# Kernel tuning notes

Measured on AMD Instinct MI355X. Metric: run time of the kernel, lower is better.

## Reference

```python
import jax, jax.numpy as jnp
import numpy as np

N_NODES = 100_000
N_EDGES = 3_200_000
IN_DIM, HID, OUT_DIM = 500, 16, 500


def _gcn_conv(x, W, b, src, dst, norm, n_nodes):
    # PyG GCNConv: h = X W; out[dst] += norm * h[src]; out += b
    h = x @ W                                   # [N, out]
    msg = h[src] * norm[:, None]                # [E+N, out]
    out = jax.ops.segment_sum(msg, dst, num_segments=n_nodes)
    return out + b


def setup_inputs() -> dict:
    key = jax.random.key(0)
    ks = jax.random.split(key, 8)
    x = jax.random.normal(ks[0], (N_NODES, IN_DIM), dtype=jnp.float32)
    edge_index = jax.random.randint(ks[1], (2, N_EDGES), 0, N_NODES, dtype=jnp.int32)
    # Glorot-ish init scale for the linear weights
    W1 = jax.random.normal(ks[2], (IN_DIM, HID), dtype=jnp.float32) * (1.0 / np.sqrt(IN_DIM))
    b1 = jnp.zeros((HID,), dtype=jnp.float32)
    W2 = jax.random.normal(ks[3], (HID, HID), dtype=jnp.float32) * (1.0 / np.sqrt(HID))
    b2 = jnp.zeros((HID,), dtype=jnp.float32)
    W3 = jax.random.normal(ks[4], (HID, OUT_DIM), dtype=jnp.float32) * (1.0 / np.sqrt(HID))
    b3 = jnp.zeros((OUT_DIM,), dtype=jnp.float32)
    return {"x": x, "edge_index": edge_index, "W1": W1, "b1": b1,
            "W2": W2, "b2": b2, "W3": W3, "b3": b3}


def reference(x, edge_index, W1, b1, W2, b2, W3, b3):
    n = x.shape[0]
    loops = jnp.arange(n, dtype=edge_index.dtype)
    src = jnp.concatenate([edge_index[0], loops])  # add self-loops
    dst = jnp.concatenate([edge_index[1], loops])
    # symmetric normalization: deg over (A + I), norm_e = d^-1/2[src] * d^-1/2[dst]
    deg = jax.ops.segment_sum(jnp.ones_like(src, dtype=x.dtype), dst, num_segments=n)
    dis = jnp.where(deg > 0, jax.lax.rsqrt(deg), 0.0)
    norm = dis[src] * dis[dst]

    h = _gcn_conv(x, W1, b1, src, dst, norm, n)
    h = jax.nn.relu(h)
    h = _gcn_conv(h, W2, b2, src, dst, norm, n)
    h = jax.nn.relu(h)
    out = _gcn_conv(h, W3, b3, src, dst, norm, n)
    return out
```

## Files before the change

### kernel.cpp

```cpp
#include <hip/hip_runtime.h>

#define N_NODES 100000
#define N_EDGES 3200000
#define IN_DIM 500
#define HID 16
#define OUT_DIM 500

__global__ void k_deg(const int* __restrict__ dst, int* __restrict__ cnt, int E) {
    int e = blockIdx.x * blockDim.x + threadIdx.x;
    if (e < E) atomicAdd(&cnt[dst[e]], 1);
}

__global__ void k_dis(const int* __restrict__ cnt, float* __restrict__ dis, int n) {
    int i = blockIdx.x * blockDim.x + threadIdx.x;
    if (i < n) dis[i] = rsqrtf((float)(cnt[i] + 1));
}

__global__ __launch_bounds__(1024) void k_scanA(const int* __restrict__ cnt,
                                                int* __restrict__ rowptr,
                                                int* __restrict__ bsum) {
    __shared__ int sh[1024];
    int t = threadIdx.x;
    int i = blockIdx.x * 1024 + t;
    int v = (i < N_NODES) ? cnt[i] : 0;
    sh[t] = v;
    __syncthreads();
    for (int off = 1; off < 1024; off <<= 1) {
        int tmp = (t >= off) ? sh[t - off] : 0;
        __syncthreads();
        sh[t] += tmp;
        __syncthreads();
    }
    if (i < N_NODES) rowptr[i] = sh[t] - v;
    if (t == 1023) bsum[blockIdx.x] = sh[1023];
}

__global__ __launch_bounds__(128) void k_scanB(int* __restrict__ bsum, int nb) {
    __shared__ int sh[128];
    int t = threadIdx.x;
    int v = (t < nb) ? bsum[t] : 0;
    sh[t] = v;
    __syncthreads();
    for (int off = 1; off < 128; off <<= 1) {
        int tmp = (t >= off) ? sh[t - off] : 0;
        __syncthreads();
        sh[t] += tmp;
        __syncthreads();
    }
    if (t < nb) bsum[t] = sh[t] - v;
}

__global__ void k_scanC(int* __restrict__ rowptr, const int* __restrict__ bsum) {
    int i = blockIdx.x * blockDim.x + threadIdx.x;
    if (i < N_NODES) rowptr[i] += bsum[i >> 10];
    if (i == 0) rowptr[N_NODES] = N_EDGES;
}

__global__ void k_fill(const int* __restrict__ src, const int* __restrict__ dst,
                       const int* __restrict__ rowptr, int* __restrict__ cursor,
                       int* __restrict__ csr, int E) {
    int e = blockIdx.x * blockDim.x + threadIdx.x;
    if (e < E) {
        int d = dst[e];
        int p = rowptr[d] + atomicAdd(&cursor[d], 1);
        csr[p] = src[e];
    }
}

__global__ __launch_bounds__(256) void k_mm1(const float* __restrict__ x,
                                             const float* __restrict__ W,
                                             const float* __restrict__ dis,
                                             float* __restrict__ hp) {
    int row = blockIdx.x * 256 + threadIdx.x;
    if (row >= N_NODES) return;
    const float4* xr = (const float4*)(x + (size_t)row * IN_DIM);
    float acc[HID];
#pragma unroll
    for (int j = 0; j < HID; ++j) acc[j] = 0.0f;

    float4 A[8], B[8];
#pragma unroll
    for (int m = 0; m < 8; ++m) A[m] = xr[m];

#define MM1_GROUP(buf, g)                                                 \
    {                                                                     \
        const float* Wg = W + (size_t)(g) * 32 * HID;                     \
        _Pragma("unroll") for (int m = 0; m < 8; ++m) {                   \
            float4 a = buf[m];                                            \
            _Pragma("unroll") for (int j = 0; j < HID; ++j) {             \
                acc[j] += a.x * Wg[(4 * m + 0) * HID + j]                 \
                        + a.y * Wg[(4 * m + 1) * HID + j]                 \
                        + a.z * Wg[(4 * m + 2) * HID + j]                 \
                        + a.w * Wg[(4 * m + 3) * HID + j];                \
            }                                                             \
        }                                                                 \
    }

    for (int gg = 0; gg < 7; ++gg) {
        int g0 = 2 * gg;
#pragma unroll
        for (int m = 0; m < 8; ++m) B[m] = xr[8 * (g0 + 1) + m];
        MM1_GROUP(A, g0);
#pragma unroll
        for (int m = 0; m < 8; ++m) A[m] = xr[8 * (g0 + 2) + m];
        MM1_GROUP(B, g0 + 1);
    }
    MM1_GROUP(A, 14);
#pragma unroll
    for (int m = 0; m < 5; ++m) {
        float4 a = xr[120 + m];
        const float* Wg = W + (size_t)(480 + 4 * m) * HID;
#pragma unroll
        for (int j = 0; j < HID; ++j) {
            acc[j] += a.x * Wg[j] + a.y * Wg[HID + j] +
                      a.z * Wg[2 * HID + j] + a.w * Wg[3 * HID + j];
        }
    }
#undef MM1_GROUP

    float di = dis[row];
    float4* hr = (float4*)(hp + (size_t)row * HID);
#pragma unroll
    for (int q = 0; q < 4; ++q)
        hr[q] = make_float4(di * acc[4 * q + 0], di * acc[4 * q + 1],
                            di * acc[4 * q + 2], di * acc[4 * q + 3]);
}

__global__ __launch_bounds__(256) void k_mm2(const float* __restrict__ o,
                                             const float* __restrict__ W,
                                             const float* __restrict__ dis,
                                             float* __restrict__ hp) {
    int row = blockIdx.x * 256 + threadIdx.x;
    if (row >= N_NODES) return;
    const float4* orow = (const float4*)(o + (size_t)row * HID);
    float av[HID];
#pragma unroll
    for (int q = 0; q < 4; ++q) {
        float4 a = orow[q];
        av[4 * q + 0] = a.x; av[4 * q + 1] = a.y;
        av[4 * q + 2] = a.z; av[4 * q + 3] = a.w;
    }
    float acc[HID];
#pragma unroll
    for (int j = 0; j < HID; ++j) acc[j] = 0.0f;
#pragma unroll
    for (int k = 0; k < HID; ++k) {
#pragma unroll
        for (int j = 0; j < HID; ++j) acc[j] += av[k] * W[k * HID + j];
    }
    float di = dis[row];
    float4* hr = (float4*)(hp + (size_t)row * HID);
#pragma unroll
    for (int q = 0; q < 4; ++q)
        hr[q] = make_float4(di * acc[4 * q + 0], di * acc[4 * q + 1],
                            di * acc[4 * q + 2], di * acc[4 * q + 3]);
}

__global__ void k_scale(const float* __restrict__ o, const float* __restrict__ dis,
                        float* __restrict__ hp) {
    int t = blockIdx.x * blockDim.x + threadIdx.x;
    if (t < N_NODES * HID) hp[t] = dis[t >> 4] * o[t];
}

template <int RELU>
__global__ __launch_bounds__(256) void k_gather(const int* __restrict__ rowptr,
                                                const int* __restrict__ csr,
                                                const float* __restrict__ dis,
                                                const float* __restrict__ hp,
                                                const float* __restrict__ b,
                                                float* __restrict__ o) {
    int g = threadIdx.x >> 4;
    int f = threadIdx.x & 15;
    int d = blockIdx.x * 16 + g;
    int start = rowptr[d];
    int end = rowptr[d + 1];
    float s = 0.0f;
    for (int e0 = start; e0 < end; e0 += 16) {
        int idx = e0 + f;
        int sid = (idx < end) ? csr[idx] : 0;
        int m = end - e0;
        if (m > 16) m = 16;
        for (int j = 0; j < m; ++j) {
            int sj = __shfl(sid, j, 16);
            s += hp[(size_t)sj * HID + f];
        }
    }
    float di = dis[d];
    float v = di * (s + hp[(size_t)d * HID + f]);
    if (RELU) {
        v += b[f];
        v = v > 0.0f ? v : 0.0f;
    }
    o[(size_t)d * HID + f] = v;
}

__global__ __launch_bounds__(256) void k_mm3(const float* __restrict__ a,
                                             const float* __restrict__ W,
                                             const float* __restrict__ b,
                                             float* __restrict__ out) {
    __shared__ float Ws[HID * OUT_DIM];
    __shared__ float bs[OUT_DIM];
    for (int t = threadIdx.x; t < HID * OUT_DIM; t += 256) Ws[t] = W[t];
    for (int t = threadIdx.x; t < OUT_DIM; t += 256) bs[t] = b[t];
    __syncthreads();
    int ct = threadIdx.x & 127;
    int rt = threadIdx.x >> 7;
    int r0 = blockIdx.x * 8 + rt * 4;
    float areg[4][16];
#pragma unroll
    for (int rr = 0; rr < 4; ++rr) {
        const float4* ap = (const float4*)(a + (size_t)(r0 + rr) * HID);
        float4 v0 = ap[0], v1 = ap[1], v2 = ap[2], v3 = ap[3];
        areg[rr][0] = v0.x;  areg[rr][1] = v0.y;  areg[rr][2] = v0.z;  areg[rr][3] = v0.w;
        areg[rr][4] = v1.x;  areg[rr][5] = v1.y;  areg[rr][6] = v1.z;  areg[rr][7] = v1.w;
        areg[rr][8] = v2.x;  areg[rr][9] = v2.y;  areg[rr][10] = v2.z; areg[rr][11] = v2.w;
        areg[rr][12] = v3.x; areg[rr][13] = v3.y; areg[rr][14] = v3.z; areg[rr][15] = v3.w;
    }
    if (ct >= 125) return;
    int j0 = ct * 4;
    float acc[4][4];
#pragma unroll
    for (int rr = 0; rr < 4; ++rr) {
        acc[rr][0] = bs[j0];
        acc[rr][1] = bs[j0 + 1];
        acc[rr][2] = bs[j0 + 2];
        acc[rr][3] = bs[j0 + 3];
    }
#pragma unroll
    for (int k = 0; k < HID; ++k) {
        float4 w = *(const float4*)&Ws[k * OUT_DIM + j0];
#pragma unroll
        for (int rr = 0; rr < 4; ++rr) {
            acc[rr][0] += areg[rr][k] * w.x;
            acc[rr][1] += areg[rr][k] * w.y;
            acc[rr][2] += areg[rr][k] * w.z;
            acc[rr][3] += areg[rr][k] * w.w;
        }
    }
#pragma unroll
    for (int rr = 0; rr < 4; ++rr) {
        float4 r = make_float4(acc[rr][0], acc[rr][1], acc[rr][2], acc[rr][3]);
        *(float4*)&out[(size_t)(r0 + rr) * OUT_DIM + j0] = r;
    }
}

extern "C" void kernel_launch(void* const* d_in, const int* in_sizes, int n_in,
                              void* d_out, int out_size, void* d_ws, size_t ws_size,
                              hipStream_t stream) {
    const float* x  = (const float*)d_in[0];
    const int* ei   = (const int*)d_in[1];
    const float* W1 = (const float*)d_in[2];
    const float* b1 = (const float*)d_in[3];
    const float* W2 = (const float*)d_in[4];
    const float* b2 = (const float*)d_in[5];
    const float* W3 = (const float*)d_in[6];
    const float* b3 = (const float*)d_in[7];
    float* out = (float*)d_out;

    const int* src = ei;
    const int* dst = ei + N_EDGES;

    char* w = (char*)d_ws;
    float* dis    = (float*)(w);
    int*   cnt    = (int*)(w + 401408);
    int*   rowptr = (int*)(w + 802816);
    int*   bsum   = (int*)(w + 1205248);
    int*   csr    = (int*)(w + 1205760);
    float* hp     = (float*)(w + 14005760);
    float* o      = (float*)(w + 20405760);

    const int B = 256;
    int gN   = (N_NODES + B - 1) / B;
    int gE   = (N_EDGES + B - 1) / B;
    int gNH  = (N_NODES * HID + B - 1) / B;
    int gG   = N_NODES / 16;
    int gMM3 = N_NODES / 8;
    int gScanA = (N_NODES + 1023) / 1024;

    hipMemsetAsync(cnt, 0, N_NODES * sizeof(int), stream);
    k_deg<<<gE, B, 0, stream>>>(dst, cnt, N_EDGES);
    k_dis<<<gN, B, 0, stream>>>(cnt, dis, N_NODES);

    k_scanA<<<gScanA, 1024, 0, stream>>>(cnt, rowptr, bsum);
    k_scanB<<<1, 128, 0, stream>>>(bsum, gScanA);
    k_scanC<<<gN, B, 0, stream>>>(rowptr, bsum);
    hipMemsetAsync(cnt, 0, N_NODES * sizeof(int), stream);
    k_fill<<<gE, B, 0, stream>>>(src, dst, rowptr, cnt, csr, N_EDGES);

    k_mm1<<<gN, B, 0, stream>>>(x, W1, dis, hp);
    k_gather<1><<<gG, B, 0, stream>>>(rowptr, csr, dis, hp, b1, o);

    k_mm2<<<gN, B, 0, stream>>>(o, W2, dis, hp);
    k_gather<1><<<gG, B, 0, stream>>>(rowptr, csr, dis, hp, b2, o);

    k_scale<<<gNH, B, 0, stream>>>(o, dis, hp);
    k_gather<0><<<gG, B, 0, stream>>>(rowptr, csr, dis, hp, b3, o);
    k_mm3<<<gMM3, B, 0, stream>>>(o, W3, b3, out);
}
```

Before: 937.2 us.

## Build CSR with a two-pass bucketed sort instead of global atomic scatter

```diff
diff --git a/kernel.cpp b/kernel.cpp
--- a/kernel.cpp
+++ b/kernel.cpp
@@ -5,6 +5,10 @@
 #define IN_DIM 500
 #define HID 16
 #define OUT_DIM 500
+
+#define BSHIFT 9
+#define NBUCK 196
+#define PLACE_CAP 24576
 
 __global__ void k_deg(const int* __restrict__ dst, int* __restrict__ cnt, int E) {
     int e = blockIdx.x * blockDim.x + threadIdx.x;
@@ -56,14 +60,86 @@
     if (i == 0) rowptr[N_NODES] = N_EDGES;
 }
 
-__global__ void k_fill(const int* __restrict__ src, const int* __restrict__ dst,
-                       const int* __restrict__ rowptr, int* __restrict__ cursor,
-                       int* __restrict__ csr, int E) {
-    int e = blockIdx.x * blockDim.x + threadIdx.x;
-    if (e < E) {
-        int d = dst[e];
-        int p = rowptr[d] + atomicAdd(&cursor[d], 1);
-        csr[p] = src[e];
+__global__ void k_initcur(const int* __restrict__ rowptr, int* __restrict__ cur) {
+    int b = blockIdx.x * blockDim.x + threadIdx.x;
+    if (b < NBUCK) cur[b] = rowptr[b << BSHIFT];
+}
+
+__global__ __launch_bounds__(512) void k_bin(const int* __restrict__ src,
+                                             const int* __restrict__ dst,
+                                             int* __restrict__ cur,
+                                             unsigned* __restrict__ ebin, int E) {
+    __shared__ int hist[NBUCK];
+    __shared__ int gbase[NBUCK];
+    int t = threadIdx.x;
+    for (int i = t; i < NBUCK; i += 512) hist[i] = 0;
+    __syncthreads();
+    int base = blockIdx.x * 8192;
+    unsigned epack[16];
+    unsigned lpack[16];
+#pragma unroll
+    for (int q = 0; q < 16; ++q) {
+        int e = base + q * 512 + t;
+        unsigned ep = 0, lp = 0xFFFFFFFFu;
+        if (e < E) {
+            int s = src[e];
+            int d = dst[e];
+            int b = d >> BSHIFT;
+            int loc = atomicAdd(&hist[b], 1);
+            ep = ((unsigned)s << BSHIFT) | (unsigned)(d & 511);
+            lp = ((unsigned)loc << 8) | (unsigned)b;
+        }
+        epack[q] = ep;
+        lpack[q] = lp;
+    }
+    __syncthreads();
+    for (int i = t; i < NBUCK; i += 512)
+        gbase[i] = hist[i] ? atomicAdd(&cur[i], hist[i]) : 0;
+    __syncthreads();
+#pragma unroll
+    for (int q = 0; q < 16; ++q) {
+        if (lpack[q] != 0xFFFFFFFFu) {
+            int b = (int)(lpack[q] & 255u);
+            int loc = (int)(lpack[q] >> 8);
+            ebin[gbase[b] + loc] = epack[q];
+        }
+    }
+}
+
+__global__ __launch_bounds__(1024) void k_place(const int* __restrict__ rowptr,
+                                                const unsigned* __restrict__ ebin,
+                                                int* __restrict__ csr,
+                                                int* __restrict__ cnt) {
+    __shared__ int stage[PLACE_CAP];
+    __shared__ int rloc[513];
+    __shared__ int lcur[512];
+    int b = blockIdx.x;
+    int n0 = b << BSHIFT;
+    int n1 = n0 + 512;
+    if (n1 > N_NODES) n1 = N_NODES;
+    int nn = n1 - n0;
+    int t = threadIdx.x;
+    int base = rowptr[n0];
+    for (int i = t; i <= nn; i += 1024) rloc[i] = rowptr[n0 + i] - base;
+    for (int i = t; i < nn; i += 1024) lcur[i] = 0;
+    __syncthreads();
+    int size = rloc[nn];
+    if (size <= PLACE_CAP) {
+        for (int i = t; i < size; i += 1024) {
+            unsigned p = ebin[base + i];
+            int dlow = (int)(p & 511u);
+            int pos = atomicAdd(&lcur[dlow], 1);
+            stage[rloc[dlow] + pos] = (int)(p >> BSHIFT);
+        }
+        __syncthreads();
+        for (int i = t; i < size; i += 1024) csr[base + i] = stage[i];
+    } else {
+        for (int i = t; i < size; i += 1024) {
+            unsigned p = ebin[base + i];
+            int d = n0 + (int)(p & 511u);
+            int pos = rowptr[d] + atomicAdd(&cnt[d], 1);
+            csr[pos] = (int)(p >> BSHIFT);
+        }
     }
 }
 
@@ -261,13 +337,15 @@
     const int* dst = ei + N_EDGES;
 
     char* w = (char*)d_ws;
-    float* dis    = (float*)(w);
-    int*   cnt    = (int*)(w + 401408);
-    int*   rowptr = (int*)(w + 802816);
-    int*   bsum   = (int*)(w + 1205248);
-    int*   csr    = (int*)(w + 1205760);
-    float* hp     = (float*)(w + 14005760);
-    float* o      = (float*)(w + 20405760);
+    float* dis      = (float*)(w);
+    int*   cnt      = (int*)(w + 401408);
+    int*   cur      = (int*)(w + 801408);
+    int*   rowptr   = (int*)(w + 802816);
+    int*   bsum     = (int*)(w + 1205248);
+    int*   csr      = (int*)(w + 1205760);
+    float* hp       = (float*)(w + 14005760);
+    float* o        = (float*)(w + 20405760);
+    unsigned* ebin  = (unsigned*)(w + 14005760);
 
     const int B = 256;
     int gN   = (N_NODES + B - 1) / B;
@@ -276,6 +354,7 @@
     int gG   = N_NODES / 16;
     int gMM3 = N_NODES / 8;
     int gScanA = (N_NODES + 1023) / 1024;
+    int gBin = (N_EDGES + 8191) / 8192;
 
     hipMemsetAsync(cnt, 0, N_NODES * sizeof(int), stream);
     k_deg<<<gE, B, 0, stream>>>(dst, cnt, N_EDGES);
@@ -284,8 +363,10 @@
     k_scanA<<<gScanA, 1024, 0, stream>>>(cnt, rowptr, bsum);
     k_scanB<<<1, 128, 0, stream>>>(bsum, gScanA);
     k_scanC<<<gN, B, 0, stream>>>(rowptr, bsum);
+    k_initcur<<<1, 256, 0, stream>>>(rowptr, cur);
+    k_bin<<<gBin, 512, 0, stream>>>(src, dst, cur, ebin, N_EDGES);
     hipMemsetAsync(cnt, 0, N_NODES * sizeof(int), stream);
-    k_fill<<<gE, B, 0, stream>>>(src, dst, rowptr, cnt, csr, N_EDGES);
+    k_place<<<NBUCK, 1024, 0, stream>>>(rowptr, ebin, csr, cnt);
 
     k_mm1<<<gN, B, 0, stream>>>(x, W1, dis, hp);
     k_gather<1><<<gG, B, 0, stream>>>(rowptr, csr, dis, hp, b1, o);
```

Measured after the change: 825.3 us. -11.9%, faster.
